# Performance work log

Hardware: AMD Instinct MI355X
Metric: run time of the kernel (lower is better)

Reference implementation:

```python
import jax, jax.numpy as jnp
import numpy as np

MARGIN = 0.1
LAMBDA_EFFECT = 0.5

B, T_V, K, T_S = 32, 8192, 64, 128


def setup_inputs() -> dict:
    key = jax.random.key(0)
    k1, k2, k3, k4, k5 = jax.random.split(key, 5)
    pred_orig = jax.random.normal(k1, (B, T_V), dtype=jnp.float32)
    pred_intervened = jax.random.normal(k2, (K, B, T_V), dtype=jnp.float32)
    intervened_indices = jax.random.randint(k3, (K,), 0, T_S, dtype=jnp.int32)
    # GT alignment mask: sparse-ish binary alignment between frames and sentences
    gt_mask = jax.random.bernoulli(k4, 0.2, (B, T_V, T_S)).astype(jnp.int32)
    # prefix-valid video mask: valid length per batch in [T_V//2, T_V]
    lengths = jax.random.randint(k5, (B,), T_V // 2, T_V + 1, dtype=jnp.int32)
    mask_video = (jnp.arange(T_V, dtype=jnp.int32)[None, :] < lengths[:, None]).astype(jnp.int32)
    return {
        "pred_orig": pred_orig,
        "pred_intervened": pred_intervened,
        "intervened_indices": intervened_indices,
        "gt_mask": gt_mask,
        "mask_video": mask_video,
    }


def reference(pred_orig, pred_intervened, intervened_indices, gt_mask, mask_video):
    # pred_orig: [B,T], pred_intervened: [K,B,T], gt_mask: [B,T,S], mask_video: [B,T]
    prob_orig = jax.nn.sigmoid(pred_orig)                 # [B,T]
    prob_int = jax.nn.sigmoid(pred_intervened)            # [K,B,T]
    effect = jnp.abs(prob_orig[None, :, :] - prob_int)    # [K,B,T]

    valid = mask_video.astype(bool)                       # [B,T] (prefix mask == :T_v_valid slice)
    # gather intervened sentence columns: [B,T,K] -> [K,B,T]
    gt_sel = jnp.transpose(gt_mask[:, :, intervened_indices], (2, 0, 1))

    aligned = (gt_sel > 0) & valid[None]                  # [K,B,T]
    non_aligned = (gt_sel == 0) & valid[None]             # [K,B,T]

    cnt_a = aligned.sum(axis=-1)                          # [K,B]
    cnt_n = non_aligned.sum(axis=-1)                      # [K,B]

    ea = jnp.sum(effect * aligned, axis=-1) / jnp.maximum(cnt_a, 1)
    en = jnp.sum(effect * non_aligned, axis=-1) / jnp.maximum(cnt_n, 1)

    per_pair = jnp.where((cnt_a > 0) & (cnt_n > 0),
                         jax.nn.relu(MARGIN - (ea - en)),
                         jnp.zeros_like(ea))
    num_interventions = pred_orig.shape[0] * pred_intervened.shape[0]
    alignment_consistency = per_pair.sum() / max(num_interventions, 1)
    total_intervention_loss = alignment_consistency * LAMBDA_EFFECT
    return alignment_consistency, total_intervention_loss
```

## Files before the change

kernel.cpp:

```cpp
#include <hip/hip_runtime.h>
#include <cstdint>

#define BB 32
#define TV 8192
#define KK 64
#define TS 128
#define MARGIN_F 0.1f
#define LAMBDA_F 0.5f

typedef unsigned long long u64;
typedef unsigned int u32;

static constexpr int KB_PAIRS = KK * BB;
static constexpr int W32_PER_B = TV / 32;
static constexpr int W64_PER_B = TV / 64;


__global__ __launch_bounds__(128, 4) void plane_kernel(
    const int* __restrict__ idx, const int* __restrict__ gt,
    const int* __restrict__ mv, u32* __restrict__ vbit, u32* __restrict__ pl,
    int* __restrict__ len, int* __restrict__ mw) {
  const int lane = threadIdx.x & 63;
  const int h = threadIdx.x >> 6;
  const int blk = blockIdx.x;
  const int b = blk >> 7;
  const int g = blk & 127;
  const int w32 = g * 2 + h;
  const int grow = b * TV + g * 64 + h * 32;

  const int mvv = (lane < 32) ? mv[grow + lane] : 0;
  const u32 V = (u32)__ballot(mvv != 0);
  if (lane == 0) {
    vbit[b * W32_PER_B + w32] = V;
    if (V) {
      atomicAdd(&len[b], __popc(V));
      atomicMax(&mw[b], w32);
    }
  }

  u32 plane = 0;
  if (V) {
    const int c = idx[lane];
    const int csel = c & 3, csh = c >> 2;
    const int4* rowp = (const int4*)(gt + (size_t)grow * TS);
#pragma unroll
    for (int ch = 0; ch < 16; ++ch) {
      const int4 v = rowp[ch * 64 + lane];
      const u64 b0 = __ballot(v.x > 0);
      const u64 b1 = __ballot(v.y > 0);
      const u64 b2 = __ballot(v.z > 0);
      const u64 b3 = __ballot(v.w > 0);
      const u64 sel =
          (csel == 0) ? b0 : (csel == 1) ? b1 : (csel == 2) ? b2 : b3;
      plane |= (u32)((sel >> csh) & 1ull) << (2 * ch);
      plane |= (u32)((sel >> (32 + csh)) & 1ull) << (2 * ch + 1);
    }
    plane &= V;
  }
  pl[((size_t)(b * KK + lane) * W64_PER_B + g) * 2 + h] = plane;
}

__global__ __launch_bounds__(256, 4) void reduce_kernel(
    const float* __restrict__ po, const float* __restrict__ pi,
    const u32* __restrict__ vbit, const u32* __restrict__ pl,
    const int* __restrict__ mw,
    float* __restrict__ gsa, float* __restrict__ gsv,
    float* __restrict__ gca) {
  const int tid = threadIdx.x;
  const int lane = tid & 63;
  const int w = tid >> 6;
  const int kb = blockIdx.x;
  const int b = kb & (BB - 1);
  const int k = kb >> 5;
  const u64* plrow = (const u64*)pl + (size_t)(b * KK + k) * W64_PER_B;
  const u64* vrow = (const u64*)vbit + (size_t)b * W64_PER_B;
  const float* pirow = pi + (size_t)kb * TV;
  const float* porow = po + (size_t)b * TV;

  __shared__ float rs[4][2];
  __shared__ int rca;
  if (tid == 0) rca = 0;
  __syncthreads();

  const int nch = min(8, (mw[b] + 32) >> 5);
  const int sh = (tid & 15) * 4;
  float sa = 0.f, sv = 0.f;
#pragma unroll 2
  for (int c = 0; c < nch; ++c) {
    const int t = c * 1024 + tid * 4;
    const int widx = t >> 6;
    const u64 vw = vrow[widx];
    const u32 vb4 = (u32)((vw >> sh) & 15ull);
    if (vb4) {
      const u64 aw = plrow[widx];
      const u32 ab4 = (u32)((aw >> sh) & 15ull);
      const float4 x = *(const float4*)(pirow + t);
      const float4 p = *(const float4*)(porow + t);
      const float e0 =
          fabsf(__fdividef(1.f, 1.f + __expf(-p.x)) -
                __fdividef(1.f, 1.f + __expf(-x.x)));
      const float e1 =
          fabsf(__fdividef(1.f, 1.f + __expf(-p.y)) -
                __fdividef(1.f, 1.f + __expf(-x.y)));
      const float e2 =
          fabsf(__fdividef(1.f, 1.f + __expf(-p.z)) -
                __fdividef(1.f, 1.f + __expf(-x.z)));
      const float e3 =
          fabsf(__fdividef(1.f, 1.f + __expf(-p.w)) -
                __fdividef(1.f, 1.f + __expf(-x.w)));
      if (vb4 & 1u) sv += e0;
      if (vb4 & 2u) sv += e1;
      if (vb4 & 4u) sv += e2;
      if (vb4 & 8u) sv += e3;
      if (ab4 & 1u) sa += e0;
      if (ab4 & 2u) sa += e1;
      if (ab4 & 4u) sa += e2;
      if (ab4 & 8u) sa += e3;
    }
  }
#pragma unroll
  for (int off = 32; off; off >>= 1) {
    sa += __shfl_xor(sa, off);
    sv += __shfl_xor(sv, off);
  }
  if (lane == 0) {
    rs[w][0] = sa;
    rs[w][1] = sv;
  }
  if (tid < W64_PER_B) atomicAdd(&rca, __popcll(plrow[tid]));
  __syncthreads();
  if (tid == 0) {
    gsa[kb] = rs[0][0] + rs[1][0] + rs[2][0] + rs[3][0];
    gsv[kb] = rs[0][1] + rs[1][1] + rs[2][1] + rs[3][1];
    gca[kb] = (float)rca;
  }
}

__global__ __launch_bounds__(256) void fin_kernel(
    const float* __restrict__ gsa, const float* __restrict__ gsv,
    const float* __restrict__ gca, const int* __restrict__ len,
    float* __restrict__ out) {
  float s = 0.f;
  for (int i = threadIdx.x; i < KB_PAIRS; i += 256) {
    const int b = i & (BB - 1);
    const float ca = gca[i];
    const float cn = (float)len[b] - ca;
    if (ca > 0.f && cn > 0.f) {
      const float sa = gsa[i];
      const float sv = gsv[i];
      const float d = MARGIN_F - (sa / ca - (sv - sa) / cn);
      s += d > 0.f ? d : 0.f;
    }
  }
#pragma unroll
  for (int off = 32; off > 0; off >>= 1) s += __shfl_down(s, off);
  __shared__ float ws4[4];
  if ((threadIdx.x & 63) == 0) ws4[threadIdx.x >> 6] = s;
  __syncthreads();
  if (threadIdx.x == 0) {
    const float S = ws4[0] + ws4[1] + ws4[2] + ws4[3];
    const float ac = S * (1.0f / (float)KB_PAIRS);
    out[0] = ac;
    out[1] = ac * LAMBDA_F;
  }
}

extern "C" void kernel_launch(void* const* d_in, const int* in_sizes, int n_in,
                              void* d_out, int out_size, void* d_ws, size_t ws_size,
                              hipStream_t stream) {
  const float* pred_orig = (const float*)d_in[0];
  const float* pred_int  = (const float*)d_in[1];
  const int*   idx       = (const int*)d_in[2];
  const int*   gt        = (const int*)d_in[3];
  const int*   mv        = (const int*)d_in[4];
  float* out = (float*)d_out;

  float* gsa = (float*)d_ws;
  float* gsv = gsa + KB_PAIRS;
  float* gca = gsv + KB_PAIRS;
  int*   len = (int*)(gca + KB_PAIRS);
  int*   mw  = len + BB;
  u32*   vbit = (u32*)(mw + BB);
  u32*   pl   = vbit + BB * W32_PER_B;

  hipMemsetAsync(len, 0, 2 * BB * sizeof(int), stream);
  plane_kernel<<<BB * (TV / 64), 128, 0, stream>>>(idx, gt, mv, vbit, pl, len,
                                                   mw);
  reduce_kernel<<<KB_PAIRS, 256, 0, stream>>>(pred_orig, pred_int, vbit, pl,
                                              mw, gsa, gsv, gca);
  fin_kernel<<<1, 256, 0, stream>>>(gsa, gsv, gca, len, out);
}
```

Measured before the change: 314.0 us.

## Stage gt_mask tiles into LDS via direct global-to-LDS loads for plane building

The plane kernel now processes 128-row tiles per 256-thread block. It copies the full gt_mask tile into shared memory with global_load_lds, then each lane gathers its selected column from LDS to build 32-bit alignment planes. This replaces the per-chunk ballot-and-select scheme over register loads. Tiles where every row is invalid skip the load entirely. The trade-off is 64KB of LDS per block, which lowers occupancy, and possible bank conflicts on the strided column reads.

Result: faster. 285.8 us (-9.0%).

```diff
diff --git a/kernel.cpp b/kernel.cpp
--- a/kernel.cpp
+++ b/kernel.cpp
@@ -14,50 +14,68 @@
 static constexpr int KB_PAIRS = KK * BB;
 static constexpr int W32_PER_B = TV / 32;
 static constexpr int W64_PER_B = TV / 64;
-
-
-__global__ __launch_bounds__(128, 4) void plane_kernel(
+static constexpr int ROWS = 128;
+
+
+__global__ __launch_bounds__(256, 2) void plane_kernel(
     const int* __restrict__ idx, const int* __restrict__ gt,
     const int* __restrict__ mv, u32* __restrict__ vbit, u32* __restrict__ pl,
     int* __restrict__ len, int* __restrict__ mw) {
-  const int lane = threadIdx.x & 63;
-  const int h = threadIdx.x >> 6;
+  const int tid = threadIdx.x;
+  const int lane = tid & 63;
+  const int w = tid >> 6;
   const int blk = blockIdx.x;
-  const int b = blk >> 7;
-  const int g = blk & 127;
-  const int w32 = g * 2 + h;
-  const int grow = b * TV + g * 64 + h * 32;
-
-  const int mvv = (lane < 32) ? mv[grow + lane] : 0;
-  const u32 V = (u32)__ballot(mvv != 0);
+  const int b = blk >> 6;
+  const int tile = blk & 63;
+  const int t0 = tile * ROWS;
+
+  __shared__ u32 sV[4];
+  __shared__ int gtile[ROWS * TS];
+
+  const int rbase = b * TV + t0 + 32 * w;
+  const int mvv = (lane < 32) ? mv[rbase + lane] : 0;
+  const u32 V32 = (u32)__ballot(mvv != 0);
+  const int g2 = t0 / 32 + w;
   if (lane == 0) {
-    vbit[b * W32_PER_B + w32] = V;
-    if (V) {
-      atomicAdd(&len[b], __popc(V));
-      atomicMax(&mw[b], w32);
-    }
-  }
-
+    sV[w] = V32;
+    vbit[b * W32_PER_B + g2] = V32;
+    if (V32) {
+      atomicAdd(&len[b], __popc(V32));
+      atomicMax(&mw[b], g2);
+    }
+  }
+  __syncthreads();
+
+  u32* plbase = pl + (size_t)b * KK * W32_PER_B + g2;
+
+  if ((sV[0] | sV[1] | sV[2] | sV[3]) == 0u) {
+    plbase[(size_t)lane * W32_PER_B] = 0u;
+    return;
+  }
+
+  {
+    const char* gsrc = (const char*)(gt + (size_t)(b * TV + t0) * TS);
+    char* lbase = (char*)gtile;
+#pragma unroll
+    for (int i = 0; i < 16; ++i) {
+      const int off = (w * 16 + i) * 1024;
+      __builtin_amdgcn_global_load_lds(
+          (const __attribute__((address_space(1))) u32*)(gsrc + off +
+                                                         lane * 16),
+          (__attribute__((address_space(3))) u32*)(lbase + off), 16, 0, 0);
+    }
+  }
+  __syncthreads();
+
+  const int c = idx[lane];
+  const int* col = gtile + 32 * w * TS + c;
   u32 plane = 0;
-  if (V) {
-    const int c = idx[lane];
-    const int csel = c & 3, csh = c >> 2;
-    const int4* rowp = (const int4*)(gt + (size_t)grow * TS);
-#pragma unroll
-    for (int ch = 0; ch < 16; ++ch) {
-      const int4 v = rowp[ch * 64 + lane];
-      const u64 b0 = __ballot(v.x > 0);
-      const u64 b1 = __ballot(v.y > 0);
-      const u64 b2 = __ballot(v.z > 0);
-      const u64 b3 = __ballot(v.w > 0);
-      const u64 sel =
-          (csel == 0) ? b0 : (csel == 1) ? b1 : (csel == 2) ? b2 : b3;
-      plane |= (u32)((sel >> csh) & 1ull) << (2 * ch);
-      plane |= (u32)((sel >> (32 + csh)) & 1ull) << (2 * ch + 1);
-    }
-    plane &= V;
-  }
-  pl[((size_t)(b * KK + lane) * W64_PER_B + g) * 2 + h] = plane;
+#pragma unroll
+  for (int r = 0; r < 32; ++r)
+    if (col[r * TS] > 0) plane |= 1u << r;
+  plane &= sV[w];
+
+  plbase[(size_t)lane * W32_PER_B] = plane;
 }
 
 __global__ __launch_bounds__(256, 4) void reduce_kernel(
@@ -184,8 +202,8 @@
   u32*   pl   = vbit + BB * W32_PER_B;
 
   hipMemsetAsync(len, 0, 2 * BB * sizeof(int), stream);
-  plane_kernel<<<BB * (TV / 64), 128, 0, stream>>>(idx, gt, mv, vbit, pl, len,
-                                                   mw);
+  plane_kernel<<<BB * (TV / ROWS), 256, 0, stream>>>(idx, gt, mv, vbit, pl,
+                                                     len, mw);
   reduce_kernel<<<KB_PAIRS, 256, 0, stream>>>(pred_orig, pred_int, vbit, pl,
                                               mw, gsa, gsv, gca);
   fin_kernel<<<1, 256, 0, stream>>>(gsa, gsv, gca, len, out);
```
